# Kernel tuning notes

Hardware: AMD Instinct MI355X
Metric: run time of the kernel (lower is better)

The kernel has to match this reference:

```python
import jax, jax.numpy as jnp
import numpy as np

B, S, ENC, DEC, ATTN, H = 256, 512, 256, 256, 128, 48

def setup_inputs() -> dict:
    key = jax.random.key(0)
    ks = jax.random.split(key, 12)
    n = jax.random.normal
    return {
        'enc_outputs': n(ks[0], (B, S, ENC), jnp.float32),
        'h0': n(ks[1], (B, DEC), jnp.float32),
        'c0': n(ks[2], (B, DEC), jnp.float32),
        'W_enc': n(ks[3], (ENC, ATTN), jnp.float32) * 0.05,
        'W_dec': n(ks[4], (DEC, ATTN), jnp.float32) * 0.05,
        'v': n(ks[5], (ATTN,), jnp.float32) * 0.05,
        'W_ih': n(ks[6], (4 * DEC, 1 + ENC), jnp.float32) * 0.05,
        'W_hh': n(ks[7], (4 * DEC, DEC), jnp.float32) * 0.05,
        'b_ih': n(ks[8], (4 * DEC,), jnp.float32) * 0.05,
        'b_hh': n(ks[9], (4 * DEC,), jnp.float32) * 0.05,
        'W_out': n(ks[10], (DEC,), jnp.float32) * 0.05,
        'b_out': n(ks[11], (1,), jnp.float32) * 0.05,
    }

def reference(enc_outputs, h0, c0, W_enc, W_dec, v, W_ih, W_hh, b_ih, b_hh, W_out, b_out):
    # Precompute encoder projection (constant across timesteps; same math as per-step).
    enc_proj = jnp.einsum('bse,ea->bsa', enc_outputs, W_enc)  # [B,S,ATTN]
    batch = enc_outputs.shape[0]
    inp0 = jnp.zeros((batch, 1), enc_outputs.dtype)

    def step(carry, _):
        h, c, inp = carry
        dec_proj = h @ W_dec  # [B,ATTN]
        scores = jnp.tanh(enc_proj + dec_proj[:, None, :]) @ v  # [B,S]
        attn_w = jax.nn.softmax(scores, axis=-1)
        context = jnp.einsum('bs,bse->be', attn_w, enc_outputs)  # [B,ENC]
        rnn_in = jnp.concatenate([inp, context], axis=-1)  # [B,1+ENC]
        gates = rnn_in @ W_ih.T + b_ih + h @ W_hh.T + b_hh  # [B,4*DEC]
        i, f, g, o = jnp.split(gates, 4, axis=-1)  # PyTorch LSTMCell gate order
        c_new = jax.nn.sigmoid(f) * c + jax.nn.sigmoid(i) * jnp.tanh(g)
        h_new = jax.nn.sigmoid(o) * jnp.tanh(c_new)
        out = h_new @ W_out + b_out[0]  # [B]
        return (h_new, c_new, out[:, None]), (out, attn_w)

    _, (preds, attn_seq) = jax.lax.scan(step, (h0, c0, inp0), None, length=H)
    preds = jnp.transpose(preds, (1, 0))        # [B,H]
    attn_seq = jnp.transpose(attn_seq, (1, 0, 2))  # [B,H,S]
    return preds, attn_seq
```

## Files before the change

kernel.cpp:

```cpp
#include <hip/hip_runtime.h>
#include <stdint.h>

#define LOG2E 1.4426950408889634f
#define SCOPE __HIP_MEMORY_SCOPE_AGENT

typedef short v8s __attribute__((ext_vector_type(8)));
typedef float v4f __attribute__((ext_vector_type(4)));

__device__ __forceinline__ uint32_t bf16r(float x){
  uint32_t u = __float_as_uint(x);
  return (u + 0x7fffu + ((u >> 16) & 1u)) >> 16;
}
__device__ __forceinline__ uint32_t pack2(float lo, float hi){
  return bf16r(lo) | (bf16r(hi) << 16);
}
__device__ __forceinline__ float unlo(uint32_t u){ return __uint_as_float(u << 16); }
__device__ __forceinline__ float unhi(uint32_t u){ return __uint_as_float(u & 0xffff0000u); }

__device__ __forceinline__ float fexp2(float x){ return __builtin_amdgcn_exp2f(x); }
__device__ __forceinline__ float frcp(float x){ return __builtin_amdgcn_rcpf(x); }
__device__ __forceinline__ float ftanh(float x){
  float e = fexp2(x * (2.0f * LOG2E));
  return 1.0f - 2.0f * frcp(e + 1.0f);
}
__device__ __forceinline__ float fsig(float x){
  return frcp(1.0f + fexp2(-x * LOG2E));
}
__device__ __forceinline__ float wave_sum(float x){
  #pragma unroll
  for(int o = 32; o; o >>= 1) x += __shfl_xor(x, o, 64);
  return x;
}

__device__ __forceinline__ unsigned flag_ld(const unsigned* p){
  return __hip_atomic_load(p, __ATOMIC_RELAXED, SCOPE);
}
__device__ __forceinline__ void flag_st(unsigned* p, unsigned v){
  __hip_atomic_store(p, v, __ATOMIC_RELAXED, SCOPE);
}
__device__ __forceinline__ float ldf_c(const float* p){
  return __hip_atomic_load(p, __ATOMIC_RELAXED, SCOPE);
}
__device__ __forceinline__ void stf_c(float* p, float v){
  __hip_atomic_store(p, v, __ATOMIC_RELAXED, SCOPE);
}
__device__ __forceinline__ uint64_t ld64_c(const uint64_t* p){
  return __hip_atomic_load(p, __ATOMIC_RELAXED, SCOPE);
}
__device__ __forceinline__ void st64_c(uint64_t* p, uint64_t v){
  __hip_atomic_store(p, v, __ATOMIC_RELAXED, SCOPE);
}
__device__ __forceinline__ void st32_c(uint32_t* p, uint32_t v){
  __hip_atomic_store(p, v, __ATOMIC_RELAXED, SCOPE);
}
__device__ __forceinline__ void st16_c(unsigned short* p, unsigned short v){
  __hip_atomic_store(p, v, __ATOMIC_RELAXED, SCOPE);
}

__device__ __forceinline__ int gate_row(int jg){
  return (jg & 3) * 256 + (jg >> 6) * 16 + ((jg >> 2) & 15);
}

__global__ __launch_bounds__(256) void k_pack(const float* __restrict__ W_ih,
                                              const float* __restrict__ W_hh,
                                              const float* __restrict__ b_ih,
                                              const float* __restrict__ b_hh,
                                              const float* __restrict__ W_enc,
                                              unsigned short* __restrict__ WmT,
                                              float* __restrict__ biasc,
                                              float* __restrict__ w0v,
                                              unsigned short* __restrict__ WencTh,
                                              unsigned short* __restrict__ WencTl){
  int gid = blockIdx.x * 256 + threadIdx.x;
  if(gid < 65536){
    int jg = gid >> 6, k8 = gid & 63;
    int row = gate_row(jg);
    int k0 = k8 * 8;
    uint32_t p[4];
    #pragma unroll
    for(int mm = 0; mm < 4; ++mm){
      int ka = k0 + 2 * mm, kb = ka + 1;
      float lo = (ka < 256) ? W_ih[row * 257 + 1 + ka] : W_hh[row * 256 + (ka - 256)];
      float hi = (kb < 256) ? W_ih[row * 257 + 1 + kb] : W_hh[row * 256 + (kb - 256)];
      p[mm] = pack2(lo, hi);
    }
    *(uint4*)&WmT[(size_t)jg * 512 + k0] = make_uint4(p[0], p[1], p[2], p[3]);
    if(k8 == 0){
      biasc[jg] = b_ih[row] + b_hh[row];
      w0v[jg] = W_ih[row * 257];
    }
  } else {
    int g2 = gid - 65536;
    int k = g2 >> 7, a = g2 & 127;
    float x = W_enc[k * 128 + a];
    uint32_t hb = bf16r(x);
    WencTh[a * 256 + k] = (unsigned short)hb;
    float hv = __uint_as_float(hb << 16);
    WencTl[a * 256 + k] = (unsigned short)bf16r(x - hv);
  }
}

__global__ __launch_bounds__(256, 2) void k_enc_proj(const float* __restrict__ enc,
                                                     const unsigned short* __restrict__ WencTh,
                                                     const unsigned short* __restrict__ WencTl,
                                                     unsigned short* __restrict__ ep,
                                                     uint32_t* __restrict__ encb){
  __shared__ unsigned short Ash[128][48];
  __shared__ unsigned short Asl[128][48];
  __shared__ unsigned short Wth[128][48];
  __shared__ unsigned short Wtl[128][48];
  const int tid = threadIdx.x;
  const int b = blockIdx.x >> 2, mt = blockIdx.x & 3;
  const int lane = tid & 63, w = tid >> 6;
  const int rr = lane & 15, quad = lane >> 4;

  v4f acc[2][8];
  #pragma unroll
  for(int g = 0; g < 2; ++g)
    #pragma unroll
    for(int nt = 0; nt < 8; ++nt) acc[g][nt] = (v4f){0.f, 0.f, 0.f, 0.f};

  const float* encBase = enc + ((size_t)(b * 512 + mt * 128)) * 256;
  uint32_t* encbBase = encb + ((size_t)(b * 512 + mt * 128)) * 128;

  for(int kt = 0; kt < 8; ++kt){
    __syncthreads();
    #pragma unroll
    for(int i = 0; i < 4; ++i){
      int flat = i * 256 + tid;
      int row = flat >> 3, c4 = flat & 7;
      float4 f = *(const float4*)(encBase + (size_t)row * 256 + kt * 32 + c4 * 4);
      uint32_t hx = bf16r(f.x), hy = bf16r(f.y), hz = bf16r(f.z), hw = bf16r(f.w);
      uint2 hp = make_uint2(hx | (hy << 16), hz | (hw << 16));
      float lx = f.x - __uint_as_float(hx << 16);
      float ly = f.y - __uint_as_float(hy << 16);
      float lz = f.z - __uint_as_float(hz << 16);
      float lw = f.w - __uint_as_float(hw << 16);
      uint2 lp = make_uint2(pack2(lx, ly), pack2(lz, lw));
      *(uint2*)&Ash[row][c4 * 4] = hp;
      *(uint2*)&Asl[row][c4 * 4] = lp;
      *(uint2*)&encbBase[(size_t)row * 128 + kt * 16 + c4 * 2] = hp;
    }
    #pragma unroll
    for(int i = 0; i < 2; ++i){
      int flat = i * 256 + tid;
      int a = flat >> 2, q4 = flat & 3;
      *(uint4*)&Wth[a][q4 * 8] = *(const uint4*)(WencTh + (size_t)a * 256 + kt * 32 + q4 * 8);
      *(uint4*)&Wtl[a][q4 * 8] = *(const uint4*)(WencTl + (size_t)a * 256 + kt * 32 + q4 * 8);
    }
    __syncthreads();
    #pragma unroll
    for(int g = 0; g < 2; ++g){
      v8s ah = *(const v8s*)&Ash[32 * w + 16 * g + rr][quad * 8];
      v8s al = *(const v8s*)&Asl[32 * w + 16 * g + rr][quad * 8];
      #pragma unroll
      for(int nt = 0; nt < 8; ++nt){
        v8s bh = *(const v8s*)&Wth[nt * 16 + rr][quad * 8];
        v8s bl = *(const v8s*)&Wtl[nt * 16 + rr][quad * 8];
        acc[g][nt] = __builtin_amdgcn_mfma_f32_16x16x32_bf16(ah, bh, acc[g][nt], 0, 0, 0);
        acc[g][nt] = __builtin_amdgcn_mfma_f32_16x16x32_bf16(al, bh, acc[g][nt], 0, 0, 0);
        acc[g][nt] = __builtin_amdgcn_mfma_f32_16x16x32_bf16(ah, bl, acc[g][nt], 0, 0, 0);
      }
    }
  }
  #pragma unroll
  for(int g = 0; g < 2; ++g){
    int s0 = 128 * mt + 32 * w + 16 * g + quad * 4;
    #pragma unroll
    for(int nt = 0; nt < 8; ++nt){
      int a = nt * 16 + rr;
      uint2 pp = make_uint2(pack2(acc[g][nt][0], acc[g][nt][1]),
                            pack2(acc[g][nt][2], acc[g][nt][3]));
      *(uint2*)&ep[((size_t)b * 128 + a) * 512 + s0] = pp;
    }
  }
}

__global__ __launch_bounds__(512) void k_zero(unsigned* __restrict__ fl){
  fl[threadIdx.x] = 0u;
}

__global__ __launch_bounds__(512, 2) void k_steps(
    const uint32_t* __restrict__ encb, const unsigned short* __restrict__ ep,
    const unsigned short* __restrict__ WmT, const float* __restrict__ biasc,
    const float* __restrict__ w0v, const float* __restrict__ Wdec,
    const float* __restrict__ Wout, const float* __restrict__ h0,
    const float* __restrict__ c0, const float* __restrict__ v,
    const float* __restrict__ b_out, unsigned* __restrict__ flagA,
    unsigned* __restrict__ flagB, float* __restrict__ predf,
    float* __restrict__ dpp, float* __restrict__ predp,
    unsigned short* __restrict__ xcat2, float* __restrict__ out)
{
  __shared__ __align__(16) unsigned short WT[64][520];
  __shared__ __align__(16) unsigned short AT[16][520];
  __shared__ float WdecL[16][128];
  __shared__ float gact[64][20];
  __shared__ float hl[16][17];
  __shared__ float dpf[128];
  __shared__ float vl[128];
  __shared__ float scp[512][9];
  __shared__ float attn_l[512];
  __shared__ float ctxp[16][256];
  __shared__ float ctxf[256];
  __shared__ float red2[8];
  __shared__ float hf[256];
  __shared__ float dppart[4][128];
  __shared__ float biasL[64], w0L[64], WoutL[16], predfL[16];
  __shared__ float sB;

  const int tid = threadIdx.x, b = blockIdx.x;
  const int lane = tid & 63, wid = tid >> 6;
  const int m16 = (b >> 4) << 4;
  const int n = b & 15;

  {
    const uint4* src = (const uint4*)(WmT + (size_t)(n * 64) * 512);
    #pragma unroll
    for(int i = 0; i < 8; ++i){
      int flat = i * 512 + tid;
      int r = flat >> 6, q = flat & 63;
      *(uint4*)&WT[r][q * 8] = src[r * 64 + q];
    }
    const float4* wsrc = (const float4*)(Wdec + (size_t)(n * 16) * 128);
    int r2 = tid >> 5, q2 = tid & 31;
    *(float4*)&WdecL[r2][q2 * 4] = wsrc[r2 * 32 + q2];
    if(tid < 64){ biasL[tid] = biasc[n * 64 + tid]; w0L[tid] = w0v[n * 64 + tid]; }
    if(tid < 16) WoutL[tid] = Wout[n * 16 + tid];
    if(tid < 128) vl[tid] = v[tid];
    if(tid == 0){ sB = b_out[0]; stf_c(&predf[b], 0.f); }
  }
  float c_reg = 0.f;
  if(tid < 256){
    int bl = tid >> 4, dl = tid & 15;
    c_reg = c0[(size_t)(m16 + bl) * 256 + n * 16 + dl];
    float hv = h0[(size_t)b * 256 + tid];
    hf[tid] = hv;
    st16_c(&xcat2[(size_t)b * 512 + 256 + tid], (unsigned short)bf16r(hv));
  }
  __syncthreads();
  {
    int a = tid & 127, p = tid >> 7;
    float s = 0.f;
    const float* wd = Wdec + (size_t)(p * 64) * 128 + a;
    #pragma unroll 8
    for(int d = 0; d < 64; ++d) s += hf[p * 64 + d] * wd[(size_t)d * 128];
    dppart[p][a] = s;
  }
  __syncthreads();
  if(tid < 128) dpf[tid] = dppart[0][tid] + dppart[1][tid] + dppart[2][tid] + dppart[3][tid];
  __syncthreads();

  const uint4* ep4 = (const uint4*)(ep + (size_t)b * 65536);
  const uint4* eb  = (const uint4*)(encb + (size_t)b * 65536);

  #pragma unroll 1
  for(int t = 0; t < 48; ++t){
    unsigned short* xcatP = xcat2 + (size_t)(t & 1) * 131072;
    unsigned short* xcatN = xcat2 + (size_t)((t + 1) & 1) * 131072;

    if(t > 0){
      if(tid < 16){
        unsigned want = (unsigned)t;
        while(flag_ld(&flagB[m16 + tid]) < want) __builtin_amdgcn_s_sleep(1);
      }
      __syncthreads();
      if(tid < 128){
        float s = 0.f;
        #pragma unroll
        for(int nn = 0; nn < 16; ++nn) s += ldf_c(&dpp[((size_t)b * 16 + nn) * 128 + tid]);
        dpf[tid] = s;
      } else if(tid == 128){
        float pf = 0.f;
        #pragma unroll
        for(int nn = 0; nn < 16; ++nn) pf += ldf_c(&predp[nn * 256 + b]);
        pf += sB;
        out[b * 48 + (t - 1)] = pf;
        stf_c(&predf[b], pf);
      }
      __syncthreads();
    }

    {
      uint4 u[16];
      #pragma unroll
      for(int i = 0; i < 16; ++i) u[i] = ep4[(wid * 16 + i) * 64 + lane];
      float sc[8];
      #pragma unroll
      for(int j = 0; j < 8; ++j) sc[j] = 0.f;
      #pragma unroll
      for(int i = 0; i < 16; ++i){
        int a = wid * 16 + i;
        float dd = dpf[a], vv = vl[a];
        sc[0] += vv * ftanh(unlo(u[i].x) + dd);
        sc[1] += vv * ftanh(unhi(u[i].x) + dd);
        sc[2] += vv * ftanh(unlo(u[i].y) + dd);
        sc[3] += vv * ftanh(unhi(u[i].y) + dd);
        sc[4] += vv * ftanh(unlo(u[i].z) + dd);
        sc[5] += vv * ftanh(unhi(u[i].z) + dd);
        sc[6] += vv * ftanh(unlo(u[i].w) + dd);
        sc[7] += vv * ftanh(unhi(u[i].w) + dd);
      }
      #pragma unroll
      for(int j = 0; j < 8; ++j) scp[lane * 8 + j][wid] = sc[j];
    }
    __syncthreads();

    float wexp;
    {
      float s = 0.f;
      #pragma unroll
      for(int q = 0; q < 8; ++q) s += scp[tid][q];
      wexp = fexp2(s * LOG2E);
      float sw = wave_sum(wexp);
      if(lane == 0) red2[wid] = sw;
    }
    __syncthreads();
    {
      float L = red2[0];
      #pragma unroll
      for(int i = 1; i < 8; ++i) L += red2[i];
      float aw = wexp * frcp(L);
      attn_l[tid] = aw;
      out[12288 + (size_t)b * 24576 + t * 512 + tid] = aw;
    }
    __syncthreads();

    {
      int e4 = tid & 31, g = tid >> 5;
      float a8[8] = {0.f, 0.f, 0.f, 0.f, 0.f, 0.f, 0.f, 0.f};
      #pragma unroll 8
      for(int i = 0; i < 32; ++i){
        int s = g * 32 + i;
        float at = attn_l[s];
        uint4 uu = eb[s * 32 + e4];
        a8[0] += at * unlo(uu.x); a8[1] += at * unhi(uu.x);
        a8[2] += at * unlo(uu.y); a8[3] += at * unhi(uu.y);
        a8[4] += at * unlo(uu.z); a8[5] += at * unhi(uu.z);
        a8[6] += at * unlo(uu.w); a8[7] += at * unhi(uu.w);
      }
      #pragma unroll
      for(int j = 0; j < 8; ++j) ctxp[g][e4 * 8 + j] = a8[j];
    }
    __syncthreads();
    if(tid < 256){
      float s = 0.f;
      #pragma unroll
      for(int g = 0; g < 16; ++g) s += ctxp[g][tid];
      ctxf[tid] = s;
    }
    __syncthreads();
    if(tid < 128)
      st32_c((uint32_t*)&xcatP[(size_t)b * 512 + 2 * tid],
             pack2(ctxf[2 * tid], ctxf[2 * tid + 1]));
    __syncthreads();
    if(tid == 0) flag_st(&flagA[b], (unsigned)(t + 1));

    if(tid < 16){
      unsigned want = (unsigned)(t + 1);
      while(flag_ld(&flagA[m16 + tid]) < want) __builtin_amdgcn_s_sleep(1);
    }
    __syncthreads();
    {
      const uint64_t* asrc = (const uint64_t*)(xcatP + (size_t)m16 * 512);
      #pragma unroll
      for(int i = 0; i < 4; ++i){
        int flat = i * 512 + tid;
        int r = flat >> 7, q = flat & 127;
        *(uint64_t*)&AT[r][q * 4] = ld64_c(asrc + (size_t)r * 128 + q);
      }
      if(tid < 16) predfL[tid] = ldf_c(&predf[m16 + tid]);
    }
    __syncthreads();
    if(tid < 256){
      const int quad = (tid & 63) >> 4, rr = tid & 15;
      const int jl = (tid >> 6) * 16 + rr;
      v4f acc = {0.f, 0.f, 0.f, 0.f};
      #pragma unroll
      for(int kt = 0; kt < 16; ++kt){
        int k0 = kt * 32 + quad * 8;
        v8s av = *(const v8s*)&AT[rr][k0];
        v8s bv = *(const v8s*)&WT[jl][k0];
        acc = __builtin_amdgcn_mfma_f32_16x16x32_bf16(av, bv, acc, 0, 0, 0);
      }
      float bias = biasL[jl], w0 = w0L[jl];
      int gate = jl & 3;
      #pragma unroll
      for(int r = 0; r < 4; ++r){
        int bl = quad * 4 + r;
        float pre = acc[r] + bias + predfL[bl] * w0;
        gact[jl][bl] = (gate == 2) ? ftanh(pre) : fsig(pre);
      }
    }
    __syncthreads();
    if(tid < 256){
      int bl = tid >> 4, dl = tid & 15;
      float gi = gact[dl * 4 + 0][bl];
      float gf = gact[dl * 4 + 1][bl];
      float gg = gact[dl * 4 + 2][bl];
      float go = gact[dl * 4 + 3][bl];
      int bg = m16 + bl, dg = n * 16 + dl;
      float cn = gf * c_reg + gi * gg;
      c_reg = cn;
      float hn = go * ftanh(cn);
      st16_c(&xcatN[(size_t)bg * 512 + 256 + dg], (unsigned short)bf16r(hn));
      hl[bl][dl] = hn;
      float pp = hn * WoutL[dl];
      #pragma unroll
      for(int o = 8; o; o >>= 1) pp += __shfl_xor(pp, o, 64);
      if(dl == 0) stf_c(&predp[n * 256 + bg], pp);
    }
    __syncthreads();
    if(tid < 256){
      int bl = tid >> 4, ag = tid & 15;
      int bg = m16 + bl;
      float a0[8] = {0, 0, 0, 0, 0, 0, 0, 0};
      #pragma unroll
      for(int d = 0; d < 16; ++d){
        float hv = hl[bl][d];
        #pragma unroll
        for(int j = 0; j < 8; ++j) a0[j] += hv * WdecL[d][ag * 8 + j];
      }
      float* dst = &dpp[((size_t)bg * 16 + n) * 128 + ag * 8];
      #pragma unroll
      for(int j = 0; j < 4; ++j){
        uint64_t uu = (uint64_t)__float_as_uint(a0[2 * j]) |
                      ((uint64_t)__float_as_uint(a0[2 * j + 1]) << 32);
        st64_c((uint64_t*)(dst + 2 * j), uu);
      }
    }
    __syncthreads();
    if(tid == 0) flag_st(&flagB[b], (unsigned)(t + 1));
  }

  if(tid < 16){
    while(flag_ld(&flagB[m16 + tid]) < 48u) __builtin_amdgcn_s_sleep(1);
  }
  __syncthreads();
  if(tid == 0){
    float pf = 0.f;
    #pragma unroll
    for(int nn = 0; nn < 16; ++nn) pf += ldf_c(&predp[nn * 256 + b]);
    out[b * 48 + 47] = pf + sB;
  }
}

extern "C" void kernel_launch(void* const* d_in, const int* in_sizes, int n_in,
                              void* d_out, int out_size, void* d_ws, size_t ws_size,
                              hipStream_t stream) {
  (void)in_sizes; (void)n_in; (void)out_size; (void)ws_size;
  const float* enc  = (const float*)d_in[0];
  const float* h0   = (const float*)d_in[1];
  const float* c0   = (const float*)d_in[2];
  const float* Wenc = (const float*)d_in[3];
  const float* Wdec = (const float*)d_in[4];
  const float* v    = (const float*)d_in[5];
  const float* Wih  = (const float*)d_in[6];
  const float* Whh  = (const float*)d_in[7];
  const float* bih  = (const float*)d_in[8];
  const float* bhh  = (const float*)d_in[9];
  const float* Wout = (const float*)d_in[10];
  const float* bout = (const float*)d_in[11];
  float* out = (float*)d_out;
  uint8_t* p = (uint8_t*)d_ws;

  uint32_t* encb = (uint32_t*)p;            p += 67108864ull;
  unsigned short* ep = (unsigned short*)p;  p += 33554432ull;
  unsigned short* WmT = (unsigned short*)p; p += 1048576ull;
  float* biasc  = (float*)p;                p += 4096ull;
  float* w0v    = (float*)p;                p += 4096ull;
  unsigned short* WencTh = (unsigned short*)p; p += 131072ull;
  unsigned short* WencTl = (unsigned short*)p; p += 131072ull;
  float* dpp    = (float*)p;                p += 2097152ull;
  float* predp  = (float*)p;                p += 16384ull;
  unsigned short* xcat2 = (unsigned short*)p; p += 524288ull;

  unsigned* flagA = (unsigned*)WencTh;
  unsigned* flagB = flagA + 256;
  float*    predf = (float*)(flagA + 512);

  k_pack<<<dim3(384), dim3(256), 0, stream>>>(Wih, Whh, bih, bhh, Wenc, WmT, biasc, w0v,
                                              WencTh, WencTl);
  k_enc_proj<<<dim3(1024), dim3(256), 0, stream>>>(enc, WencTh, WencTl, ep, encb);
  k_zero<<<dim3(1), dim3(512), 0, stream>>>(flagA);
  k_steps<<<dim3(256), dim3(512), 0, stream>>>(encb, ep, WmT, biasc, w0v, Wdec, Wout,
                                               h0, c0, v, bout, flagA, flagB, predf,
                                               dpp, predp, xcat2, out);
}
```

Measured before the change: 1.416 ms.

## Split LSTM gate GEMM to overlap hidden-state half with attention and trim syncs

The gate MFMA is split in two. The hidden-state half (K=256..511) is computed before the attention scoring, right after waiting on flagB, so it overlaps the attention phase. Only the context half runs after the flagA barrier, which shortens the critical path between blocks. It also prefetches encoder-projection loads before the flag wait, software-pipelines the context loads into double-buffered registers, and fuses the context reduction and bf16 pack. The attention-weight global store moves after the flag publish, and an LDS round-trip plus sync is replaced with shuffles for the dec_proj partials. The trade-off is higher register pressure from holding acc and u[16] live across phases.

```diff
diff --git a/kernel.cpp b/kernel.cpp
--- a/kernel.cpp
+++ b/kernel.cpp
@@ -195,13 +195,11 @@
   __shared__ __align__(16) unsigned short AT[16][520];
   __shared__ float WdecL[16][128];
   __shared__ float gact[64][20];
-  __shared__ float hl[16][17];
   __shared__ float dpf[128];
   __shared__ float vl[128];
-  __shared__ float scp[512][9];
+  __shared__ float scp[512][10];
   __shared__ float attn_l[512];
-  __shared__ float ctxp[16][256];
-  __shared__ float ctxf[256];
+  __shared__ float ctxp[16][8][33];
   __shared__ float red2[8];
   __shared__ float hf[256];
   __shared__ float dppart[4][128];
@@ -228,14 +226,18 @@
     if(tid < 16) WoutL[tid] = Wout[n * 16 + tid];
     if(tid < 128) vl[tid] = v[tid];
     if(tid == 0){ sB = b_out[0]; stf_c(&predf[b], 0.f); }
+    #pragma unroll
+    for(int i = 0; i < 8; ++i){
+      int flat = i * 512 + tid;
+      int r = flat >> 8, c = flat & 255;
+      AT[r][256 + c] = (unsigned short)bf16r(h0[(size_t)(m16 + r) * 256 + c]);
+    }
   }
   float c_reg = 0.f;
   if(tid < 256){
     int bl = tid >> 4, dl = tid & 15;
     c_reg = c0[(size_t)(m16 + bl) * 256 + n * 16 + dl];
-    float hv = h0[(size_t)b * 256 + tid];
-    hf[tid] = hv;
-    st16_c(&xcat2[(size_t)b * 512 + 256 + tid], (unsigned short)bf16r(hv));
+    hf[tid] = h0[(size_t)b * 256 + tid];
   }
   __syncthreads();
   {
@@ -258,12 +260,25 @@
     unsigned short* xcatP = xcat2 + (size_t)(t & 1) * 131072;
     unsigned short* xcatN = xcat2 + (size_t)((t + 1) & 1) * 131072;
 
+    uint4 u[16];
+    #pragma unroll
+    for(int i = 0; i < 16; ++i) u[i] = ep4[(wid * 16 + i) * 64 + lane];
+
     if(t > 0){
       if(tid < 16){
         unsigned want = (unsigned)t;
         while(flag_ld(&flagB[m16 + tid]) < want) __builtin_amdgcn_s_sleep(1);
       }
       __syncthreads();
+      {
+        const uint64_t* hsrc = (const uint64_t*)(xcatP + (size_t)m16 * 512);
+        #pragma unroll
+        for(int i = 0; i < 2; ++i){
+          int flat = i * 512 + tid;
+          int r = flat >> 6, q = flat & 63;
+          *(uint64_t*)&AT[r][256 + q * 4] = ld64_c(hsrc + (size_t)r * 128 + 64 + q);
+        }
+      }
       if(tid < 128){
         float s = 0.f;
         #pragma unroll
@@ -280,10 +295,20 @@
       __syncthreads();
     }
 
+    v4f acc = {0.f, 0.f, 0.f, 0.f};
+    if(tid < 256){
+      const int q4 = (tid & 63) >> 4, rr16 = tid & 15;
+      const int jl = (tid >> 6) * 16 + rr16;
+      #pragma unroll
+      for(int kt = 8; kt < 16; ++kt){
+        int k0 = kt * 32 + q4 * 8;
+        v8s av = *(const v8s*)&AT[rr16][k0];
+        v8s bv = *(const v8s*)&WT[jl][k0];
+        acc = __builtin_amdgcn_mfma_f32_16x16x32_bf16(av, bv, acc, 0, 0, 0);
+      }
+    }
+
     {
-      uint4 u[16];
-      #pragma unroll
-      for(int i = 0; i < 16; ++i) u[i] = ep4[(wid * 16 + i) * 64 + lane];
       float sc[8];
       #pragma unroll
       for(int j = 0; j < 8; ++j) sc[j] = 0.f;
@@ -319,41 +344,73 @@
       float L = red2[0];
       #pragma unroll
       for(int i = 1; i < 8; ++i) L += red2[i];
-      float aw = wexp * frcp(L);
-      attn_l[tid] = aw;
-      out[12288 + (size_t)b * 24576 + t * 512 + tid] = aw;
+      attn_l[tid] = wexp * frcp(L);
     }
     __syncthreads();
 
     {
       int e4 = tid & 31, g = tid >> 5;
+      const uint4* ebg = eb + ((size_t)g * 32) * 32 + e4;
+      const float* al = &attn_l[g * 32];
+      uint4 ca[8], cbf[8];
       float a8[8] = {0.f, 0.f, 0.f, 0.f, 0.f, 0.f, 0.f, 0.f};
-      #pragma unroll 8
-      for(int i = 0; i < 32; ++i){
-        int s = g * 32 + i;
-        float at = attn_l[s];
-        uint4 uu = eb[s * 32 + e4];
-        a8[0] += at * unlo(uu.x); a8[1] += at * unhi(uu.x);
-        a8[2] += at * unlo(uu.y); a8[3] += at * unhi(uu.y);
-        a8[4] += at * unlo(uu.z); a8[5] += at * unhi(uu.z);
-        a8[6] += at * unlo(uu.w); a8[7] += at * unhi(uu.w);
-      }
-      #pragma unroll
-      for(int j = 0; j < 8; ++j) ctxp[g][e4 * 8 + j] = a8[j];
-    }
-    __syncthreads();
-    if(tid < 256){
-      float s = 0.f;
-      #pragma unroll
-      for(int g = 0; g < 16; ++g) s += ctxp[g][tid];
-      ctxf[tid] = s;
-    }
-    __syncthreads();
-    if(tid < 128)
-      st32_c((uint32_t*)&xcatP[(size_t)b * 512 + 2 * tid],
-             pack2(ctxf[2 * tid], ctxf[2 * tid + 1]));
+      #pragma unroll
+      for(int i = 0; i < 8; ++i) ca[i] = ebg[i * 32];
+      #pragma unroll
+      for(int i = 0; i < 8; ++i) cbf[i] = ebg[(8 + i) * 32];
+      #pragma unroll
+      for(int i = 0; i < 8; ++i){
+        float at = al[i];
+        a8[0] += at * unlo(ca[i].x); a8[1] += at * unhi(ca[i].x);
+        a8[2] += at * unlo(ca[i].y); a8[3] += at * unhi(ca[i].y);
+        a8[4] += at * unlo(ca[i].z); a8[5] += at * unhi(ca[i].z);
+        a8[6] += at * unlo(ca[i].w); a8[7] += at * unhi(ca[i].w);
+      }
+      #pragma unroll
+      for(int i = 0; i < 8; ++i) ca[i] = ebg[(16 + i) * 32];
+      #pragma unroll
+      for(int i = 0; i < 8; ++i){
+        float at = al[8 + i];
+        a8[0] += at * unlo(cbf[i].x); a8[1] += at * unhi(cbf[i].x);
+        a8[2] += at * unlo(cbf[i].y); a8[3] += at * unhi(cbf[i].y);
+        a8[4] += at * unlo(cbf[i].z); a8[5] += at * unhi(cbf[i].z);
+        a8[6] += at * unlo(cbf[i].w); a8[7] += at * unhi(cbf[i].w);
+      }
+      #pragma unroll
+      for(int i = 0; i < 8; ++i) cbf[i] = ebg[(24 + i) * 32];
+      #pragma unroll
+      for(int i = 0; i < 8; ++i){
+        float at = al[16 + i];
+        a8[0] += at * unlo(ca[i].x); a8[1] += at * unhi(ca[i].x);
+        a8[2] += at * unlo(ca[i].y); a8[3] += at * unhi(ca[i].y);
+        a8[4] += at * unlo(ca[i].z); a8[5] += at * unhi(ca[i].z);
+        a8[6] += at * unlo(ca[i].w); a8[7] += at * unhi(ca[i].w);
+      }
+      #pragma unroll
+      for(int i = 0; i < 8; ++i){
+        float at = al[24 + i];
+        a8[0] += at * unlo(cbf[i].x); a8[1] += at * unhi(cbf[i].x);
+        a8[2] += at * unlo(cbf[i].y); a8[3] += at * unhi(cbf[i].y);
+        a8[4] += at * unlo(cbf[i].z); a8[5] += at * unhi(cbf[i].z);
+        a8[6] += at * unlo(cbf[i].w); a8[7] += at * unhi(cbf[i].w);
+      }
+      #pragma unroll
+      for(int j = 0; j < 8; ++j) ctxp[g][j][e4] = a8[j];
+    }
+    __syncthreads();
+    if(tid < 128){
+      int e0 = 2 * tid, e1 = e0 + 1;
+      float s0 = 0.f, s1 = 0.f;
+      #pragma unroll
+      for(int g2 = 0; g2 < 16; ++g2){
+        s0 += ctxp[g2][e0 & 7][e0 >> 3];
+        s1 += ctxp[g2][e1 & 7][e1 >> 3];
+      }
+      st32_c((uint32_t*)&xcatP[(size_t)b * 512 + 2 * tid], pack2(s0, s1));
+    }
     __syncthreads();
     if(tid == 0) flag_st(&flagA[b], (unsigned)(t + 1));
+    out[12288 + (size_t)b * 24576 + t * 512 + tid] = attn_l[tid];
 
     if(tid < 16){
       unsigned want = (unsigned)(t + 1);
@@ -361,24 +418,23 @@
     }
     __syncthreads();
     {
-      const uint64_t* asrc = (const uint64_t*)(xcatP + (size_t)m16 * 512);
-      #pragma unroll
-      for(int i = 0; i < 4; ++i){
+      const uint64_t* csrc = (const uint64_t*)(xcatP + (size_t)m16 * 512);
+      #pragma unroll
+      for(int i = 0; i < 2; ++i){
         int flat = i * 512 + tid;
-        int r = flat >> 7, q = flat & 127;
-        *(uint64_t*)&AT[r][q * 4] = ld64_c(asrc + (size_t)r * 128 + q);
+        int r = flat >> 6, q = flat & 63;
+        *(uint64_t*)&AT[r][q * 4] = ld64_c(csrc + (size_t)r * 128 + q);
       }
       if(tid < 16) predfL[tid] = ldf_c(&predf[m16 + tid]);
     }
     __syncthreads();
     if(tid < 256){
-      const int quad = (tid & 63) >> 4, rr = tid & 15;
-      const int jl = (tid >> 6) * 16 + rr;
-      v4f acc = {0.f, 0.f, 0.f, 0.f};
-      #pragma unroll
-      for(int kt = 0; kt < 16; ++kt){
-        int k0 = kt * 32 + quad * 8;
-        v8s av = *(const v8s*)&AT[rr][k0];
+      const int q4 = (tid & 63) >> 4, rr16 = tid & 15;
+      const int jl = (tid >> 6) * 16 + rr16;
+      #pragma unroll
+      for(int kt = 0; kt < 8; ++kt){
+        int k0 = kt * 32 + q4 * 8;
+        v8s av = *(const v8s*)&AT[rr16][k0];
         v8s bv = *(const v8s*)&WT[jl][k0];
         acc = __builtin_amdgcn_mfma_f32_16x16x32_bf16(av, bv, acc, 0, 0, 0);
       }
@@ -386,7 +442,7 @@
       int gate = jl & 3;
       #pragma unroll
       for(int r = 0; r < 4; ++r){
-        int bl = quad * 4 + r;
+        int bl = q4 * 4 + r;
         float pre = acc[r] + bias + predfL[bl] * w0;
         gact[jl][bl] = (gate == 2) ? ftanh(pre) : fsig(pre);
       }
@@ -403,24 +459,18 @@
       c_reg = cn;
       float hn = go * ftanh(cn);
       st16_c(&xcatN[(size_t)bg * 512 + 256 + dg], (unsigned short)bf16r(hn));
-      hl[bl][dl] = hn;
       float pp = hn * WoutL[dl];
       #pragma unroll
       for(int o = 8; o; o >>= 1) pp += __shfl_xor(pp, o, 64);
       if(dl == 0) stf_c(&predp[n * 256 + bg], pp);
-    }
-    __syncthreads();
-    if(tid < 256){
-      int bl = tid >> 4, ag = tid & 15;
-      int bg = m16 + bl;
       float a0[8] = {0, 0, 0, 0, 0, 0, 0, 0};
       #pragma unroll
       for(int d = 0; d < 16; ++d){
-        float hv = hl[bl][d];
+        float hv = __shfl(hn, (lane & 48) + d, 64);
         #pragma unroll
-        for(int j = 0; j < 8; ++j) a0[j] += hv * WdecL[d][ag * 8 + j];
-      }
-      float* dst = &dpp[((size_t)bg * 16 + n) * 128 + ag * 8];
+        for(int j = 0; j < 8; ++j) a0[j] += hv * WdecL[d][dl * 8 + j];
+      }
+      float* dst = &dpp[((size_t)bg * 16 + n) * 128 + dl * 8];
       #pragma unroll
       for(int j = 0; j < 4; ++j){
         uint64_t uu = (uint64_t)__float_as_uint(a0[2 * j]) |
```

After: 3.915 ms. 176% more time.

## Compute attention context with MFMA on transposed bf16 encoder and split gate GEMM

Applied to the files above, without the earlier changes.

The encoder projection kernel now writes a transposed bf16 copy of the encoder outputs (E-major). The step kernel uses it to compute the context vector with bf16 MFMA, splitting the attention weights into hi and lo bf16 parts, in place of the scalar FMA loop and shared-memory reductions. The W_hh·h half of the gate GEMM is issued before the attention phase, overlapping with the score loads, so only the context half stays on the post-barrier critical path. The dec projection uses shuffles instead of a shared-memory round trip, which removes several barriers per step, and the score scratch layout is changed to reduce LDS use. The encoder values are still rounded to bf16, and the attention weights get a two-term split to keep precision.

```diff
diff --git a/kernel.cpp b/kernel.cpp
--- a/kernel.cpp
+++ b/kernel.cpp
@@ -48,9 +48,6 @@
   return __hip_atomic_load(p, __ATOMIC_RELAXED, SCOPE);
 }
 __device__ __forceinline__ void st64_c(uint64_t* p, uint64_t v){
-  __hip_atomic_store(p, v, __ATOMIC_RELAXED, SCOPE);
-}
-__device__ __forceinline__ void st32_c(uint32_t* p, uint32_t v){
   __hip_atomic_store(p, v, __ATOMIC_RELAXED, SCOPE);
 }
 __device__ __forceinline__ void st16_c(unsigned short* p, unsigned short v){
@@ -104,7 +101,7 @@
                                                      const unsigned short* __restrict__ WencTh,
                                                      const unsigned short* __restrict__ WencTl,
                                                      unsigned short* __restrict__ ep,
-                                                     uint32_t* __restrict__ encb){
+                                                     unsigned short* __restrict__ encbT){
   __shared__ unsigned short Ash[128][48];
   __shared__ unsigned short Asl[128][48];
   __shared__ unsigned short Wth[128][48];
@@ -121,7 +118,6 @@
     for(int nt = 0; nt < 8; ++nt) acc[g][nt] = (v4f){0.f, 0.f, 0.f, 0.f};
 
   const float* encBase = enc + ((size_t)(b * 512 + mt * 128)) * 256;
-  uint32_t* encbBase = encb + ((size_t)(b * 512 + mt * 128)) * 128;
 
   for(int kt = 0; kt < 8; ++kt){
     __syncthreads();
@@ -139,7 +135,6 @@
       uint2 lp = make_uint2(pack2(lx, ly), pack2(lz, lw));
       *(uint2*)&Ash[row][c4 * 4] = hp;
       *(uint2*)&Asl[row][c4 * 4] = lp;
-      *(uint2*)&encbBase[(size_t)row * 128 + kt * 16 + c4 * 2] = hp;
     }
     #pragma unroll
     for(int i = 0; i < 2; ++i){
@@ -162,6 +157,18 @@
         acc[g][nt] = __builtin_amdgcn_mfma_f32_16x16x32_bf16(ah, bl, acc[g][nt], 0, 0, 0);
       }
     }
+    {
+      unsigned short* ebT = encbT + ((size_t)(b * 256 + kt * 32)) * 512 + mt * 128;
+      #pragma unroll
+      for(int i2 = 0; i2 < 2; ++i2){
+        int flat = i2 * 256 + tid;
+        int e_loc = flat & 31, sc = flat >> 5;
+        unsigned short tmp[8];
+        #pragma unroll
+        for(int i = 0; i < 8; ++i) tmp[i] = Ash[sc * 8 + i][e_loc];
+        *(uint4*)&ebT[(size_t)e_loc * 512 + sc * 8] = *(uint4*)tmp;
+      }
+    }
   }
   #pragma unroll
   for(int g = 0; g < 2; ++g){
@@ -181,7 +188,7 @@
 }
 
 __global__ __launch_bounds__(512, 2) void k_steps(
-    const uint32_t* __restrict__ encb, const unsigned short* __restrict__ ep,
+    const unsigned short* __restrict__ encbT, const unsigned short* __restrict__ ep,
     const unsigned short* __restrict__ WmT, const float* __restrict__ biasc,
     const float* __restrict__ w0v, const float* __restrict__ Wdec,
     const float* __restrict__ Wout, const float* __restrict__ h0,
@@ -195,21 +202,20 @@
   __shared__ __align__(16) unsigned short AT[16][520];
   __shared__ float WdecL[16][128];
   __shared__ float gact[64][20];
-  __shared__ float hl[16][17];
   __shared__ float dpf[128];
   __shared__ float vl[128];
-  __shared__ float scp[512][9];
-  __shared__ float attn_l[512];
-  __shared__ float ctxp[16][256];
-  __shared__ float ctxf[256];
+  __shared__ float scp[64][65];
   __shared__ float red2[8];
   __shared__ float hf[256];
   __shared__ float dppart[4][128];
+  __shared__ __align__(16) unsigned short abfh[512];
+  __shared__ __align__(16) unsigned short abfl[512];
   __shared__ float biasL[64], w0L[64], WoutL[16], predfL[16];
   __shared__ float sB;
 
   const int tid = threadIdx.x, b = blockIdx.x;
   const int lane = tid & 63, wid = tid >> 6;
+  const int quad = lane >> 4, rr = lane & 15;
   const int m16 = (b >> 4) << 4;
   const int n = b & 15;
 
@@ -228,14 +234,18 @@
     if(tid < 16) WoutL[tid] = Wout[n * 16 + tid];
     if(tid < 128) vl[tid] = v[tid];
     if(tid == 0){ sB = b_out[0]; stf_c(&predf[b], 0.f); }
+    #pragma unroll
+    for(int i = 0; i < 8; ++i){
+      int flat = i * 512 + tid;
+      int r = flat >> 8, c = flat & 255;
+      AT[r][256 + c] = (unsigned short)bf16r(h0[(size_t)(m16 + r) * 256 + c]);
+    }
   }
   float c_reg = 0.f;
   if(tid < 256){
     int bl = tid >> 4, dl = tid & 15;
     c_reg = c0[(size_t)(m16 + bl) * 256 + n * 16 + dl];
-    float hv = h0[(size_t)b * 256 + tid];
-    hf[tid] = hv;
-    st16_c(&xcat2[(size_t)b * 512 + 256 + tid], (unsigned short)bf16r(hv));
+    hf[tid] = h0[(size_t)b * 256 + tid];
   }
   __syncthreads();
   {
@@ -251,7 +261,6 @@
   __syncthreads();
 
   const uint4* ep4 = (const uint4*)(ep + (size_t)b * 65536);
-  const uint4* eb  = (const uint4*)(encb + (size_t)b * 65536);
 
   #pragma unroll 1
   for(int t = 0; t < 48; ++t){
@@ -264,6 +273,15 @@
         while(flag_ld(&flagB[m16 + tid]) < want) __builtin_amdgcn_s_sleep(1);
       }
       __syncthreads();
+      {
+        const uint64_t* hsrc = (const uint64_t*)(xcatP + (size_t)m16 * 512);
+        #pragma unroll
+        for(int i = 0; i < 2; ++i){
+          int flat = i * 512 + tid;
+          int r = flat >> 6, q = flat & 63;
+          *(uint64_t*)&AT[r][256 + q * 4] = ld64_c(hsrc + (size_t)r * 128 + 64 + q);
+        }
+      }
       if(tid < 128){
         float s = 0.f;
         #pragma unroll
@@ -280,10 +298,23 @@
       __syncthreads();
     }
 
+    uint4 u[16];
+    #pragma unroll
+    for(int i = 0; i < 16; ++i) u[i] = ep4[(wid * 16 + i) * 64 + lane];
+
+    v4f acc = {0.f, 0.f, 0.f, 0.f};
+    if(tid < 256){
+      const int jl = (tid >> 6) * 16 + rr;
+      #pragma unroll
+      for(int kt = 8; kt < 16; ++kt){
+        int k0 = kt * 32 + quad * 8;
+        v8s av = *(const v8s*)&AT[rr][k0];
+        v8s bv = *(const v8s*)&WT[jl][k0];
+        acc = __builtin_amdgcn_mfma_f32_16x16x32_bf16(av, bv, acc, 0, 0, 0);
+      }
+    }
+
     {
-      uint4 u[16];
-      #pragma unroll
-      for(int i = 0; i < 16; ++i) u[i] = ep4[(wid * 16 + i) * 64 + lane];
       float sc[8];
       #pragma unroll
       for(int j = 0; j < 8; ++j) sc[j] = 0.f;
@@ -301,7 +332,7 @@
         sc[7] += vv * ftanh(unhi(u[i].w) + dd);
       }
       #pragma unroll
-      for(int j = 0; j < 8; ++j) scp[lane * 8 + j][wid] = sc[j];
+      for(int j = 0; j < 8; ++j) scp[j * 8 + wid][lane] = sc[j];
     }
     __syncthreads();
 
@@ -309,7 +340,7 @@
     {
       float s = 0.f;
       #pragma unroll
-      for(int q = 0; q < 8; ++q) s += scp[tid][q];
+      for(int q = 0; q < 8; ++q) s += scp[(tid & 7) * 8 + q][tid >> 3];
       wexp = fexp2(s * LOG2E);
       float sw = wave_sum(wexp);
       if(lane == 0) red2[wid] = sw;
@@ -320,38 +351,34 @@
       #pragma unroll
       for(int i = 1; i < 8; ++i) L += red2[i];
       float aw = wexp * frcp(L);
-      attn_l[tid] = aw;
+      uint32_t ah = bf16r(aw);
+      abfh[tid] = (unsigned short)ah;
+      abfl[tid] = (unsigned short)bf16r(aw - __uint_as_float(ah << 16));
       out[12288 + (size_t)b * 24576 + t * 512 + tid] = aw;
     }
     __syncthreads();
 
     {
-      int e4 = tid & 31, g = tid >> 5;
-      float a8[8] = {0.f, 0.f, 0.f, 0.f, 0.f, 0.f, 0.f, 0.f};
-      #pragma unroll 8
-      for(int i = 0; i < 32; ++i){
-        int s = g * 32 + i;
-        float at = attn_l[s];
-        uint4 uu = eb[s * 32 + e4];
-        a8[0] += at * unlo(uu.x); a8[1] += at * unhi(uu.x);
-        a8[2] += at * unlo(uu.y); a8[3] += at * unhi(uu.y);
-        a8[4] += at * unlo(uu.z); a8[5] += at * unhi(uu.z);
-        a8[6] += at * unlo(uu.w); a8[7] += at * unhi(uu.w);
-      }
-      #pragma unroll
-      for(int j = 0; j < 8; ++j) ctxp[g][e4 * 8 + j] = a8[j];
-    }
-    __syncthreads();
-    if(tid < 256){
-      float s = 0.f;
-      #pragma unroll
-      for(int g = 0; g < 16; ++g) s += ctxp[g][tid];
-      ctxf[tid] = s;
-    }
-    __syncthreads();
-    if(tid < 128)
-      st32_c((uint32_t*)&xcatP[(size_t)b * 512 + 2 * tid],
-             pack2(ctxf[2 * tid], ctxf[2 * tid + 1]));
+      const unsigned short* eT =
+          encbT + ((size_t)(b * 256) + wid * 32 + rr) * 512 + quad * 8;
+      v4f ca = {0.f, 0.f, 0.f, 0.f}, cb = {0.f, 0.f, 0.f, 0.f};
+      #pragma unroll 4
+      for(int kt = 0; kt < 16; ++kt){
+        int k0 = kt * 32;
+        v8s avh = *(const v8s*)&abfh[k0 + quad * 8];
+        v8s avl = *(const v8s*)&abfl[k0 + quad * 8];
+        v8s bv0 = *(const v8s*)(eT + k0);
+        v8s bv1 = *(const v8s*)(eT + 16 * 512 + k0);
+        ca = __builtin_amdgcn_mfma_f32_16x16x32_bf16(avh, bv0, ca, 0, 0, 0);
+        ca = __builtin_amdgcn_mfma_f32_16x16x32_bf16(avl, bv0, ca, 0, 0, 0);
+        cb = __builtin_amdgcn_mfma_f32_16x16x32_bf16(avh, bv1, cb, 0, 0, 0);
+        cb = __builtin_amdgcn_mfma_f32_16x16x32_bf16(avl, bv1, cb, 0, 0, 0);
+      }
+      if(quad == 0){
+        st16_c(&xcatP[(size_t)b * 512 + wid * 32 + rr], (unsigned short)bf16r(ca[0]));
+        st16_c(&xcatP[(size_t)b * 512 + wid * 32 + 16 + rr], (unsigned short)bf16r(cb[0]));
+      }
+    }
     __syncthreads();
     if(tid == 0) flag_st(&flagA[b], (unsigned)(t + 1));
 
@@ -361,22 +388,20 @@
     }
     __syncthreads();
     {
-      const uint64_t* asrc = (const uint64_t*)(xcatP + (size_t)m16 * 512);
-      #pragma unroll
-      for(int i = 0; i < 4; ++i){
+      const uint64_t* csrc = (const uint64_t*)(xcatP + (size_t)m16 * 512);
+      #pragma unroll
+      for(int i = 0; i < 2; ++i){
         int flat = i * 512 + tid;
-        int r = flat >> 7, q = flat & 127;
-        *(uint64_t*)&AT[r][q * 4] = ld64_c(asrc + (size_t)r * 128 + q);
+        int r = flat >> 6, q = flat & 63;
+        *(uint64_t*)&AT[r][q * 4] = ld64_c(csrc + (size_t)r * 128 + q);
       }
       if(tid < 16) predfL[tid] = ldf_c(&predf[m16 + tid]);
     }
     __syncthreads();
     if(tid < 256){
-      const int quad = (tid & 63) >> 4, rr = tid & 15;
       const int jl = (tid >> 6) * 16 + rr;
-      v4f acc = {0.f, 0.f, 0.f, 0.f};
-      #pragma unroll
-      for(int kt = 0; kt < 16; ++kt){
+      #pragma unroll
+      for(int kt = 0; kt < 8; ++kt){
         int k0 = kt * 32 + quad * 8;
         v8s av = *(const v8s*)&AT[rr][k0];
         v8s bv = *(const v8s*)&WT[jl][k0];
@@ -403,24 +428,18 @@
       c_reg = cn;
       float hn = go * ftanh(cn);
       st16_c(&xcatN[(size_t)bg * 512 + 256 + dg], (unsigned short)bf16r(hn));
-      hl[bl][dl] = hn;
       float pp = hn * WoutL[dl];
       #pragma unroll
       for(int o = 8; o; o >>= 1) pp += __shfl_xor(pp, o, 64);
       if(dl == 0) stf_c(&predp[n * 256 + bg], pp);
-    }
-    __syncthreads();
-    if(tid < 256){
-      int bl = tid >> 4, ag = tid & 15;
-      int bg = m16 + bl;
       float a0[8] = {0, 0, 0, 0, 0, 0, 0, 0};
       #pragma unroll
       for(int d = 0; d < 16; ++d){
-        float hv = hl[bl][d];
+        float hv = __shfl(hn, (lane & 48) + d, 64);
         #pragma unroll
-        for(int j = 0; j < 8; ++j) a0[j] += hv * WdecL[d][ag * 8 + j];
-      }
-      float* dst = &dpp[((size_t)bg * 16 + n) * 128 + ag * 8];
+        for(int j = 0; j < 8; ++j) a0[j] += hv * WdecL[d][dl * 8 + j];
+      }
+      float* dst = &dpp[((size_t)bg * 16 + n) * 128 + dl * 8];
       #pragma unroll
       for(int j = 0; j < 4; ++j){
         uint64_t uu = (uint64_t)__float_as_uint(a0[2 * j]) |
@@ -463,7 +482,7 @@
   float* out = (float*)d_out;
   uint8_t* p = (uint8_t*)d_ws;
 
-  uint32_t* encb = (uint32_t*)p;            p += 67108864ull;
+  unsigned short* encbT = (unsigned short*)p; p += 67108864ull;
   unsigned short* ep = (unsigned short*)p;  p += 33554432ull;
   unsigned short* WmT = (unsigned short*)p; p += 1048576ull;
   float* biasc  = (float*)p;                p += 4096ull;
@@ -480,9 +499,9 @@
 
   k_pack<<<dim3(384), dim3(256), 0, stream>>>(Wih, Whh, bih, bhh, Wenc, WmT, biasc, w0v,
                                               WencTh, WencTl);
-  k_enc_proj<<<dim3(1024), dim3(256), 0, stream>>>(enc, WencTh, WencTl, ep, encb);
+  k_enc_proj<<<dim3(1024), dim3(256), 0, stream>>>(enc, WencTh, WencTl, ep, encbT);
   k_zero<<<dim3(1), dim3(512), 0, stream>>>(flagA);
-  k_steps<<<dim3(256), dim3(512), 0, stream>>>(encb, ep, WmT, biasc, w0v, Wdec, Wout,
+  k_steps<<<dim3(256), dim3(512), 0, stream>>>(encbT, ep, WmT, biasc, w0v, Wdec, Wout,
                                                h0, c0, v, bout, flagA, flagB, predf,
                                                dpp, predp, xcat2, out);
 }
```

Measured after the change: 1.241 ms. 1.14x faster.
